# Kernel tuning notes

Measured on AMD Instinct MI355X. Metric: run time of the kernel, lower is better.

Reference implementation:

```python
import jax, jax.numpy as jnp
import numpy as np

HEADS, DH, M_LAND, PINV_ITERS, LN_EPS = 8, 64, 256, 6, 1e-5


def layer_norm(x, g, b):
    mu = x.mean(-1, keepdims=True)
    var = ((x - mu) ** 2).mean(-1, keepdims=True)
    return (x - mu) * jax.lax.rsqrt(var + LN_EPS) * g + b


def moore_penrose_pinv(x, iters=PINV_ITERS):
    # x: (h, m, m). Iterative Newton-Schulz style pinv (lucidrains).
    abs_x = jnp.abs(x)
    col = abs_x.sum(-1)
    row = abs_x.sum(-2)
    z = jnp.swapaxes(x, -1, -2) / (jnp.max(col) * jnp.max(row))
    I = jnp.eye(x.shape[-1], dtype=x.dtype)
    for _ in range(iters):
        xz = x @ z
        z = 0.25 * z @ (13.0 * I - xz @ (15.0 * I - xz @ (7.0 * I - xz)))
    return z


def nystrom_attention(x, qkv_w, out_w, out_b, res_w):
    # x: (n, dim). No mask, eval mode (dropout off).
    n, dim = x.shape
    pad = (-n) % M_LAND
    xp = jnp.pad(x, ((pad, 0), (0, 0)))  # pad at sequence START, as in original
    n_p = n + pad
    l = n_p // M_LAND  # tokens per landmark
    qkv = xp @ qkv_w  # (n_p, 3*h*dh)
    q, k, v = jnp.split(qkv, 3, axis=-1)
    split = lambda t: t.reshape(n_p, HEADS, DH).transpose(1, 0, 2)  # (h, n_p, dh)
    q, k, v = split(q), split(k), split(v)
    q = q * (DH ** -0.5)
    q_l = q.reshape(HEADS, M_LAND, l, DH).mean(axis=2)  # (h, m, dh)
    k_l = k.reshape(HEADS, M_LAND, l, DH).mean(axis=2)
    sim1 = jnp.einsum('hid,hjd->hij', q, k_l)    # (h, n_p, m)
    sim2 = jnp.einsum('hid,hjd->hij', q_l, k_l)  # (h, m, m)
    sim3 = jnp.einsum('hid,hjd->hij', q_l, k)    # (h, m, n_p)
    a1 = jax.nn.softmax(sim1, axis=-1)
    a2 = jax.nn.softmax(sim2, axis=-1)
    a3 = jax.nn.softmax(sim3, axis=-1)
    a2_inv = moore_penrose_pinv(a2)
    out = a1 @ (a2_inv @ (a3 @ v))  # (h, n_p, dh)
    # residual depthwise conv over sequence dim, kernel 33, per head
    res = jax.lax.conv_general_dilated(
        v[None], res_w, (1, 1), ((16, 16), (0, 0)),
        feature_group_count=HEADS, dimension_numbers=('NCHW', 'OIHW', 'NCHW'))[0]
    out = out + res
    out = out.transpose(1, 0, 2).reshape(n_p, HEADS * DH)
    out = out @ out_w + out_b
    return out[-n:]  # drop the leading pad


def ppeg(x, w7, b7, w5, b5, w3, b3, H, W):
    cls_tok, feat = x[0], x[1:]
    C = feat.shape[1]
    img = feat.T.reshape(1, C, H, W)
    def dw(w, b, p):
        y = jax.lax.conv_general_dilated(
            img, w, (1, 1), ((p, p), (p, p)),
            feature_group_count=C, dimension_numbers=('NCHW', 'OIHW', 'NCHW'))
        return y + b.reshape(1, C, 1, 1)
    out = img + dw(w7, b7, 3) + dw(w5, b5, 2) + dw(w3, b3, 1)
    out = out[0].reshape(C, H * W).T
    return jnp.concatenate([cls_tok[None], out], axis=0)


def forward(h, fc1_w, fc1_b, cls_token, l1_ln_g, l1_ln_b, l1_qkv_w, l1_out_w, l1_out_b, l1_res_w,
            conv7_w, conv7_b, conv5_w, conv5_b, conv3_w, conv3_b,
            l2_ln_g, l2_ln_b, l2_qkv_w, l2_out_w, l2_out_b, l2_res_w,
            norm_g, norm_b, fc2_w, fc2_b):
    x = jax.nn.relu(h @ fc1_w + fc1_b)  # (N, 512)
    N = x.shape[0]
    Hs = Ws = int(np.ceil(np.sqrt(N)))  # N chosen perfect square -> add_length == 0
    x = jnp.concatenate([cls_token, x], axis=0)  # (N+1, 512)
    x = x + nystrom_attention(layer_norm(x, l1_ln_g, l1_ln_b), l1_qkv_w, l1_out_w, l1_out_b, l1_res_w)
    x = ppeg(x, conv7_w, conv7_b, conv5_w, conv5_b, conv3_w, conv3_b, Hs, Ws)
    x = x + nystrom_attention(layer_norm(x, l2_ln_g, l2_ln_b), l2_qkv_w, l2_out_w, l2_out_b, l2_res_w)
    x = layer_norm(x, norm_g, norm_b)[0]  # cls token readout
    return x @ fc2_w + fc2_b  # (n_classes,)


def setup_inputs() -> dict:
    key = jax.random.key(0)
    ks = jax.random.split(key, 16)
    nrm = lambda k, s, sc=0.02: jax.random.normal(k, s, jnp.float32) * sc
    D = 512
    return {
        'h': jax.random.normal(ks[0], (16384, 2048), jnp.float32),
        'fc1_w': nrm(ks[1], (2048, D)), 'fc1_b': jnp.zeros((D,), jnp.float32),
        'cls_token': nrm(ks[2], (1, D), 1.0),
        'l1_ln_g': jnp.ones((D,), jnp.float32), 'l1_ln_b': jnp.zeros((D,), jnp.float32),
        'l1_qkv_w': nrm(ks[3], (D, 3 * D)),
        'l1_out_w': nrm(ks[4], (D, D)), 'l1_out_b': jnp.zeros((D,), jnp.float32),
        'l1_res_w': nrm(ks[5], (HEADS, 1, 33, 1), 0.05),
        'conv7_w': nrm(ks[6], (D, 1, 7, 7), 0.05), 'conv7_b': jnp.zeros((D,), jnp.float32),
        'conv5_w': nrm(ks[7], (D, 1, 5, 5), 0.05), 'conv5_b': jnp.zeros((D,), jnp.float32),
        'conv3_w': nrm(ks[8], (D, 1, 3, 3), 0.05), 'conv3_b': jnp.zeros((D,), jnp.float32),
        'l2_ln_g': jnp.ones((D,), jnp.float32), 'l2_ln_b': jnp.zeros((D,), jnp.float32),
        'l2_qkv_w': nrm(ks[9], (D, 3 * D)),
        'l2_out_w': nrm(ks[10], (D, D)), 'l2_out_b': jnp.zeros((D,), jnp.float32),
        'l2_res_w': nrm(ks[11], (HEADS, 1, 33, 1), 0.05),
        'norm_g': jnp.ones((D,), jnp.float32), 'norm_b': jnp.zeros((D,), jnp.float32),
        'fc2_w': nrm(ks[12], (D, 2)), 'fc2_b': jnp.zeros((2,), jnp.float32),
    }


def reference(h, fc1_w, fc1_b, cls_token, l1_ln_g, l1_ln_b, l1_qkv_w, l1_out_w, l1_out_b, l1_res_w,
              conv7_w, conv7_b, conv5_w, conv5_b, conv3_w, conv3_b,
              l2_ln_g, l2_ln_b, l2_qkv_w, l2_out_w, l2_out_b, l2_res_w,
              norm_g, norm_b, fc2_w, fc2_b):
    return forward(h, fc1_w, fc1_b, cls_token, l1_ln_g, l1_ln_b, l1_qkv_w, l1_out_w, l1_out_b, l1_res_w,
                   conv7_w, conv7_b, conv5_w, conv5_b, conv3_w, conv3_b,
                   l2_ln_g, l2_ln_b, l2_qkv_w, l2_out_w, l2_out_b, l2_res_w,
                   norm_g, norm_b, fc2_w, fc2_b)
```

## Files before the change

### kernel.cpp

```cpp
#include <hip/hip_runtime.h>
#include <cstddef>

#define NROWS 16385
#define NPAD  16640
#define PADT  255
#define DIM   512
#define HEADS 8
#define DH    64
#define NL    256
#define LCH   65
#define LCHUNK 52
#define KCH   320
#define SLACK 24
#define LDST  40
#define AST   72

typedef short bf16x8 __attribute__((ext_vector_type(8)));
typedef float f32x4  __attribute__((ext_vector_type(4)));

__device__ __forceinline__ float wsum(float v){
#pragma unroll
  for (int o = 32; o; o >>= 1) v += __shfl_xor(v, o);
  return v;
}
__device__ __forceinline__ float wmax(float v){
#pragma unroll
  for (int o = 32; o; o >>= 1) v = fmaxf(v, __shfl_xor(v, o));
  return v;
}
__device__ __forceinline__ float red16max(float v){
  v = fmaxf(v, __shfl_xor(v, 1));
  v = fmaxf(v, __shfl_xor(v, 2));
  v = fmaxf(v, __shfl_xor(v, 4));
  v = fmaxf(v, __shfl_xor(v, 8));
  return v;
}
__device__ __forceinline__ float red16sum(float v){
  v += __shfl_xor(v, 1);
  v += __shfl_xor(v, 2);
  v += __shfl_xor(v, 4);
  v += __shfl_xor(v, 8);
  return v;
}

__device__ __forceinline__ void split2(float x, unsigned short &h, unsigned short &l){
  unsigned ux = __float_as_uint(x);
  unsigned rh = (ux + 0x7FFFu + ((ux >> 16) & 1u)) >> 16;
  h = (unsigned short)rh;
  float fh = __uint_as_float(rh << 16);
  float r = x - fh;
  unsigned ur = __float_as_uint(r);
  unsigned rl = (ur + 0x7FFFu + ((ur >> 16) & 1u)) >> 16;
  l = (unsigned short)rl;
}
__device__ __forceinline__ float bf2f(unsigned short h){
  return __uint_as_float((unsigned)h << 16);
}

__global__ __launch_bounds__(256) void gemm64_sp_kernel(
    const unsigned short* __restrict__ Ah, const unsigned short* __restrict__ Al,
    const unsigned short* __restrict__ Bth, const unsigned short* __restrict__ Btl,
    const unsigned short* __restrict__ IBh, const unsigned short* __restrict__ IBl,
    float* __restrict__ Cf,
    unsigned short* __restrict__ Crh, unsigned short* __restrict__ Crl,
    unsigned short* __restrict__ Cth, unsigned short* __restrict__ Ctl,
    int M, int N, int K, long sA, long sB, long sC,
    float alpha, float ib)
{
  size_t zo = (size_t)blockIdx.z;
  Ah  += zo*sA; Al  += zo*sA;
  Bth += zo*sB; Btl += zo*sB;
  if (IBh){ IBh += zo*sA; IBl += zo*sA; }
  if (Cf)  Cf  += zo*sC;
  if (Crh){ Crh += zo*sC; Crl += zo*sC; }
  if (Cth){ Cth += zo*sC; Ctl += zo*sC; }
  __shared__ unsigned short LAh[64*LDST], LAl[64*LDST], LBh[64*LDST], LBl[64*LDST];
  const int t = threadIdx.x;
  const int wid = t >> 6, lane = t & 63;
  const int wr = wid >> 1, wc = wid & 1;
  const int l15 = lane & 15, kb = lane >> 4;
  const int bm = blockIdx.y << 6, bn = blockIdx.x << 6;
  const int r4 = t >> 2, kc = (t & 3) << 3;
  f32x4 acc[2][2];
#pragma unroll
  for (int i=0;i<2;++i)
#pragma unroll
    for (int j=0;j<2;++j) acc[i][j] = (f32x4){0.f,0.f,0.f,0.f};

  for (int k0 = 0; k0 < K; k0 += 32){
    __syncthreads();
    {
      int lo = r4*LDST + kc;
      *(uint4*)&LAh[lo] = *(const uint4*)&Ah[(size_t)(bm+r4)*K + k0 + kc];
      *(uint4*)&LAl[lo] = *(const uint4*)&Al[(size_t)(bm+r4)*K + k0 + kc];
      *(uint4*)&LBh[lo] = *(const uint4*)&Bth[(size_t)(bn+r4)*K + k0 + kc];
      *(uint4*)&LBl[lo] = *(const uint4*)&Btl[(size_t)(bn+r4)*K + k0 + kc];
    }
    __syncthreads();
    bf16x8 ah[2], al[2], bh[2], bl[2];
#pragma unroll
    for (int r=0;r<2;++r){
      int off = (wr*32 + r*16 + l15)*LDST + kb*8;
      ah[r] = *(const bf16x8*)&LAh[off];
      al[r] = *(const bf16x8*)&LAl[off];
    }
#pragma unroll
    for (int c2=0;c2<2;++c2){
      int off = (wc*32 + c2*16 + l15)*LDST + kb*8;
      bh[c2] = *(const bf16x8*)&LBh[off];
      bl[c2] = *(const bf16x8*)&LBl[off];
    }
#pragma unroll
    for (int r=0;r<2;++r)
#pragma unroll
      for (int c2=0;c2<2;++c2){
        acc[r][c2] = __builtin_amdgcn_mfma_f32_16x16x32_bf16(ah[r], bh[c2], acc[r][c2], 0,0,0);
        acc[r][c2] = __builtin_amdgcn_mfma_f32_16x16x32_bf16(ah[r], bl[c2], acc[r][c2], 0,0,0);
        acc[r][c2] = __builtin_amdgcn_mfma_f32_16x16x32_bf16(al[r], bh[c2], acc[r][c2], 0,0,0);
      }
  }
#pragma unroll
  for (int r=0;r<2;++r){
#pragma unroll
    for (int c2=0;c2<2;++c2){
      int col = bn + wc*32 + c2*16 + l15;
      int rb  = bm + wr*32 + r*16 + kb*4;
      float v[4];
#pragma unroll
      for (int e=0;e<4;++e){
        float x = acc[r][c2][e];
        if (ib != 0.f){
          size_t io = (size_t)(rb+e)*K + col;
          float ibv = bf2f(IBh[io]) + bf2f(IBl[io]);
          x = alpha*(ib*ibv - x);
        } else {
          x = alpha*x;
        }
        v[e] = x;
      }
      if (Cf){
#pragma unroll
        for (int e=0;e<4;++e) Cf[(size_t)(rb+e)*N + col] = v[e];
      }
      if (Crh){
#pragma unroll
        for (int e=0;e<4;++e){
          unsigned short hh, ll;
          split2(v[e], hh, ll);
          Crh[(size_t)(rb+e)*N + col] = hh;
          Crl[(size_t)(rb+e)*N + col] = ll;
        }
      }
      if (Cth){
        unsigned short h4[4], l4[4];
#pragma unroll
        for (int e=0;e<4;++e) split2(v[e], h4[e], l4[e]);
        uint2 uh, ul;
        uh.x = (unsigned)h4[0] | ((unsigned)h4[1]<<16);
        uh.y = (unsigned)h4[2] | ((unsigned)h4[3]<<16);
        ul.x = (unsigned)l4[0] | ((unsigned)l4[1]<<16);
        ul.y = (unsigned)l4[2] | ((unsigned)l4[3]<<16);
        *(uint2*)&Cth[(size_t)col*M + rb] = uh;
        *(uint2*)&Ctl[(size_t)col*M + rb] = ul;
      }
    }
  }
}

__global__ __launch_bounds__(256) void gemm_sb_kernel(
    const unsigned short* __restrict__ Ah, const unsigned short* __restrict__ Al,
    const unsigned short* __restrict__ BTh, const unsigned short* __restrict__ BTl,
    const float* __restrict__ bias, float* __restrict__ C,
    int M, int N, int K, int accum)
{
  __shared__ unsigned short LAh[128*LDST], LAl[128*LDST], LBh[128*LDST], LBl[128*LDST];
  const int t = threadIdx.x;
  const int bm = blockIdx.y << 7, bn = blockIdx.x << 7;
  const int wid = t >> 6, lane = t & 63;
  const int wr = wid >> 1, wc = wid & 1;
  const int l15 = lane & 15, kb = lane >> 4;
  const int sr = t >> 1, sc0 = (t & 1) << 4;
  f32x4 acc[4][4];
#pragma unroll
  for (int i=0;i<4;++i)
#pragma unroll
    for (int j=0;j<4;++j) acc[i][j] = (f32x4){0.f,0.f,0.f,0.f};

  const uint4 zz = make_uint4(0,0,0,0);
  for (int k0 = 0; k0 < K; k0 += 32){
    __syncthreads();
    {
      bool av = (bm + sr) < M;
      size_t ga = (size_t)(bm + sr)*K + k0 + sc0;
      uint4 a0 = av ? *(const uint4*)(Ah + ga)     : zz;
// ... 153 lines not shown
}

__global__ void att_split_kernel(const float* __restrict__ ATT,
                                 unsigned short* __restrict__ Ah,
                                 unsigned short* __restrict__ Al)
{
  size_t i4 = (size_t)blockIdx.x*256 + threadIdx.x;
  size_t e = i4*4;
  int row = (int)(e >> 9);
  float4 v = make_float4(0.f,0.f,0.f,0.f);
  if (row < NROWS) v = *(const float4*)(ATT + (size_t)PADT*DIM + e);
  unsigned short h0,l0,h1,l1,h2,l2,h3,l3;
  split2(v.x,h0,l0); split2(v.y,h1,l1); split2(v.z,h2,l2); split2(v.w,h3,l3);
  uint2 uh, ul;
  uh.x = (unsigned)h0 | ((unsigned)h1<<16); uh.y = (unsigned)h2 | ((unsigned)h3<<16);
  ul.x = (unsigned)l0 | ((unsigned)l1<<16); ul.y = (unsigned)l2 | ((unsigned)l3<<16);
  *(uint2*)(Ah + e) = uh;
  *(uint2*)(Al + e) = ul;
}

__global__ __launch_bounds__(256) void ln_pad_sb_kernel(
    const float* __restrict__ X, const float* __restrict__ g,
    const float* __restrict__ b, unsigned short* __restrict__ Yh,
    unsigned short* __restrict__ Yl)
{
  int p = blockIdx.x;
  int t = threadIdx.x;
  size_t base = (size_t)p*DIM;
  if (p < PADT){
    Yh[base+t] = 0; Yh[base+t+256] = 0;
    Yl[base+t] = 0; Yl[base+t+256] = 0;
    return;
  }
  const float* xr = X + (size_t)(p-PADT)*DIM;
  float x0 = xr[t], x1 = xr[t+256];
  float s = x0 + x1, sq = x0*x0 + x1*x1;
  s = wsum(s); sq = wsum(sq);
  __shared__ float rs[4], rq[4];
  if ((t&63)==0){ rs[t>>6]=s; rq[t>>6]=sq; }
  __syncthreads();
  float S = rs[0]+rs[1]+rs[2]+rs[3];
  float SQ = rq[0]+rq[1]+rq[2]+rq[3];
  float mu = S * (1.f/DIM);
  float var = SQ * (1.f/DIM) - mu*mu;
  float r = rsqrtf(var + 1e-5f);
  float y0 = (x0-mu)*r*g[t]     + b[t];
  float y1 = (x1-mu)*r*g[t+256] + b[t+256];
  unsigned short h, l;
  split2(y0, h, l); Yh[base+t] = h;     Yl[base+t] = l;
  split2(y1, h, l); Yh[base+t+256] = h; Yl[base+t+256] = l;
}

__global__ void landmarks_kernel(const float* __restrict__ QKV,
                                 float* __restrict__ QL, float* __restrict__ KL)
{
  int m = blockIdx.x, h = blockIdx.y, d = threadIdx.x;
  float sq = 0.f, sk = 0.f;
  const float* base = QKV + (size_t)(m*LCH)*1536 + (h<<6) + d;
  for (int j = 0; j < LCH; ++j){
    sq += base[0];
    sk += base[512];
    base += 1536;
  }
  QL[(((h<<8)+m)<<6) + d] = sq * (0.125f/65.f);
  KL[(((h<<8)+m)<<6) + d] = sk * (1.f/65.f);
}

__global__ void klsplit_kernel(const float* __restrict__ KL,
                               unsigned short* __restrict__ KLh,
                               unsigned short* __restrict__ KLl)
{
  int i = blockIdx.x*256 + threadIdx.x;
  unsigned short h, l;
  split2(KL[i], h, l);
  KLh[i] = h; KLl[i] = l;
}

__global__ __launch_bounds__(256) void sim2_kernel(
    const float* __restrict__ QL, const float* __restrict__ KL, float* __restrict__ A2)
{
  int m = blockIdx.x, h = blockIdx.y, n = threadIdx.x;
  __shared__ float ql[64];
  __shared__ float red[4];
  if (n < 64) ql[n] = QL[(((h<<8)+m)<<6) + n];
  __syncthreads();
  const float* kl = KL + (size_t)(((h<<8)+n)<<6);
  float s = 0.f;
#pragma unroll
  for (int d=0; d<64; ++d) s += ql[d]*kl[d];
  float mx = wmax(s);
  if ((n&63)==0) red[n>>6] = mx;
  __syncthreads();
  mx = fmaxf(fmaxf(red[0],red[1]), fmaxf(red[2],red[3]));
  float e = __expf(s - mx);
  float sm = wsum(e);
  __syncthreads();
  if ((n&63)==0) red[n>>6] = sm;
  __syncthreads();
  sm = red[0]+red[1]+red[2]+red[3];
  A2[((size_t)((h<<8)+m)<<8) + n] = e/sm;
}

__global__ void crsum_kernel(const float* __restrict__ A2, float* __restrict__ CR)
{
  int b = blockIdx.x, t = threadIdx.x;
  float v;
  if (b < 2048){
    v = fabsf(A2[((size_t)b<<8) + t]);
  } else {
    int r = b - 2048;
    int h = r >> 8, n = r & 255;
    v = fabsf(A2[((size_t)h<<16) + (t<<8) + n]);
  }
  v = wsum(v);
  __shared__ float red[4];
  if ((t&63)==0) red[t>>6]=v;
  __syncthreads();
  if (t==0) CR[b] = red[0]+red[1]+red[2]+red[3];
}
__global__ void maxprod_kernel(const float* __restrict__ CR, float* __restrict__ SCAL)
{
  int t = threadIdx.x;
  float mc = -3e38f, mr = -3e38f;
  for (int i=t; i<2048; i+=256){ mc = fmaxf(mc, CR[i]); mr = fmaxf(mr, CR[2048+i]); }
  mc = wmax(mc); mr = wmax(mr);
  __shared__ float rc[4], rr[4];
  if ((t&63)==0){ rc[t>>6]=mc; rr[t>>6]=mr; }
  __syncthreads();
  if (t==0){
    float a = fmaxf(fmaxf(rc[0],rc[1]),fmaxf(rc[2],rc[3]));
    float b = fmaxf(fmaxf(rr[0],rr[1]),fmaxf(rr[2],rr[3]));
    SCAL[0] = 1.f/(a*b);
  }
}

__global__ void tsplit_kernel(const float* __restrict__ A2, const float* __restrict__ SCAL,
                              unsigned short* __restrict__ A2h, unsigned short* __restrict__ A2l,
                              unsigned short* __restrict__ Zrh, unsigned short* __restrict__ Zrl,
                              unsigned short* __restrict__ Zth, unsigned short* __restrict__ Ztl)
{
  int idx = blockIdx.x*256 + threadIdx.x;
  int h = idx >> 16, rem = idx & 65535, m = rem >> 8, n = rem & 255;
  float a = A2[idx];
  unsigned short hh, ll;
  split2(a, hh, ll);
  A2h[idx] = hh; A2l[idx] = ll;
  float z = a * SCAL[0];
  split2(z, hh, ll);
  Zth[idx] = hh; Ztl[idx] = ll;
  size_t rmo = ((size_t)h<<16) + (n<<8) + m;
  Zrh[rmo] = hh; Zrl[rmo] = ll;
}

__global__ __launch_bounds__(256) void lattn2_kernel(
    const float* __restrict__ QKV, const float* __restrict__ QL,
    float* __restrict__ PACC, float* __restrict__ PML)
{
  const int c = blockIdx.x, lg = blockIdx.y, h = blockIdx.z;
  const int t = threadIdx.x, tx = t & 15, ty = t >> 4;
  __shared__ float QLs[64][68], KtsPs[64][68], Vs[64][68];
  {
    int r = t >> 2, c0 = (t & 3) << 4;
    const float* src = QL + (((size_t)((h << 8) + (lg << 6) + r)) << 6) + c0;
#pragma unroll
    for (int q = 0; q < 4; ++q)
      *(float4*)&QLs[r][c0 + (q<<2)] = ((const float4*)src)[q];
  }
  float M[4], L[4], acc[4][4];
#pragma unroll
  for (int i = 0; i < 4; ++i){
    M[i] = -3e38f; L[i] = 0.f;
#pragma unroll
    for (int j = 0; j < 4; ++j) acc[i][j] = 0.f;
  }
  const int key = t & 63, kd0 = (t >> 6) << 4;
  const int vr = t >> 2, vc = (t & 3) << 4;
  for (int s = 0; s < 5; ++s){
    const int j0 = c * KCH + (s << 6);
    __syncthreads();
    {
      const float* kp = QKV + (size_t)(j0 + key) * 1536 + 512 + (h << 6) + kd0;
#pragma unroll
      for (int q = 0; q < 4; ++q){
        float4 kv = ((const float4*)kp)[q];
        KtsPs[kd0 + (q<<2) + 0][key] = kv.x;
        KtsPs[kd0 + (q<<2) + 1][key] = kv.y;
        KtsPs[kd0 + (q<<2) + 2][key] = kv.z;
        KtsPs[kd0 + (q<<2) + 3][key] = kv.w;
      }
      const float* vp = QKV + (size_t)(j0 + vr) * 1536 + 1024 + (h << 6) + vc;
#pragma unroll
      for (int q = 0; q < 4; ++q)
        *(float4*)&Vs[vr][vc + (q<<2)] = ((const float4*)vp)[q];
    }
    __syncthreads();
    float sv[4][4];
#pragma unroll
    for (int i=0;i<4;++i)
#pragma unroll
      for (int j=0;j<4;++j) sv[i][j] = 0.f;
    for (int d = 0; d < 64; d += 4){
      float a[4][4], b[4][4];
#pragma unroll
      for (int i = 0; i < 4; ++i)
        *(float4*)a[i] = *(const float4*)&QLs[(ty<<2)+i][d];
#pragma unroll
      for (int dd = 0; dd < 4; ++dd)
        *(float4*)b[dd] = *(const float4*)&KtsPs[d+dd][tx<<2];
#pragma unroll
      for (int i = 0; i < 4; ++i)
#pragma unroll
        for (int dd = 0; dd < 4; ++dd){
          float av = a[i][dd];
#pragma unroll
          for (int j = 0; j < 4; ++j) sv[i][j] += av * b[dd][j];
        }
    }
#pragma unroll
    for (int i = 0; i < 4; ++i){
      float rm = fmaxf(fmaxf(sv[i][0], sv[i][1]), fmaxf(sv[i][2], sv[i][3]));
      rm = red16max(rm);
      float Mn = fmaxf(M[i], rm);
      float sc = __expf(M[i] - Mn);
      float rs = 0.f;
#pragma unroll
      for (int j = 0; j < 4; ++j){
        float p = __expf(sv[i][j] - Mn);
        sv[i][j] = p; rs += p;
      }
      rs = red16sum(rs);
      L[i] = L[i] * sc + rs;
      M[i] = Mn;
#pragma unroll
      for (int j = 0; j < 4; ++j) acc[i][j] *= sc;
    }
    __syncthreads();
#pragma unroll
    for (int i = 0; i < 4; ++i)
      *(float4*)&KtsPs[(ty<<2)+i][tx<<2] = *(float4*)sv[i];
    for (int k = 0; k < 64; k += 4){
      float a[4][4], b[4][4];
#pragma unroll
      for (int i = 0; i < 4; ++i)
        *(float4*)a[i] = *(const float4*)&KtsPs[(ty<<2)+i][k];
#pragma unroll
      for (int kk = 0; kk < 4; ++kk)
        *(float4*)b[kk] = *(const float4*)&Vs[k+kk][tx<<2];
#pragma unroll
      for (int i = 0; i < 4; ++i)
#pragma unroll
        for (int kk = 0; kk < 4; ++kk){
          float av = a[i][kk];
#pragma unroll
          for (int j = 0; j < 4; ++j) acc[i][j] += av * b[kk][j];
        }
    }
  }
  size_t base = (size_t)(c * 8 + h) * 256 + (lg << 6) + (ty << 2);
#pragma unroll
  for (int i = 0; i < 4; ++i)
    *(float4*)&PACC[(base + i) * 64 + (tx << 2)] = *(float4*)acc[i];
  if (tx == 0){
#pragma unroll
    for (int i = 0; i < 4; ++i){
      PML[(base + i) * 2 + 0] = M[i];
      PML[(base + i) * 2 + 1] = L[i];
    }
  }
}

__global__ void lattn_combine_kernel(const float* __restrict__ PACC,
                                     const float* __restrict__ PML,
                                     unsigned short* __restrict__ TMth,
                                     unsigned short* __restrict__ TMtl)
{
  int hm = blockIdx.x, d = threadIdx.x;
  int h = hm >> 8, m = hm & 255;
  float Mg = -3e38f;
#pragma unroll
  for (int c = 0; c < LCHUNK; ++c){
    size_t b = ((size_t)(c * 8 + h) * 256 + m) * 2;
    Mg = fmaxf(Mg, PML[b]);
  }
  float Sg = 0.f, o = 0.f;
#pragma unroll 4
  for (int c = 0; c < LCHUNK; ++c){
    size_t b = ((size_t)(c * 8 + h) * 256 + m) * 2;
    float e = __expf(PML[b] - Mg);
    Sg += PML[b+1] * e;
    o += PACC[((size_t)(c * 8 + h) * 256 + m) * 64 + d] * e;
  }
  unsigned short hh, ll;
  split2(o / Sg, hh, ll);
  size_t off = (size_t)h*16384 + (size_t)d*256 + m;
  TMth[off] = hh; TMtl[off] = ll;
}

__global__ __launch_bounds__(256) void attn3_kernel(
    const float* __restrict__ QKV,
    const unsigned short* __restrict__ KLh, const unsigned short* __restrict__ KLl,
    const unsigned short* __restrict__ BMth, const unsigned short* __restrict__ BMtl,
    float* __restrict__ ATT)
{
  const int qb = blockIdx.x, h = blockIdx.y;
  const int t = threadIdx.x;
  const int w = t >> 6, lane = t & 63;
  const int l15 = lane & 15, kb = lane >> 4;
  __shared__ unsigned short LQh[64*AST], LQl[64*AST];
  __shared__ unsigned short LAh[64*AST], LAl[64*AST];
  __shared__ unsigned short LPh[64*AST], LPl[64*AST];
  {
    int r = t >> 2, kc = (t & 3) << 4;
    int row = qb*64 + r; if (row > NROWS-1) row = NROWS-1;
    const float* qp = QKV + (size_t)(PADT+row)*1536 + (h<<6) + kc;
    float va[16];
    *(float4*)&va[0]  = ((const float4*)qp)[0];
    *(float4*)&va[4]  = ((const float4*)qp)[1];
    *(float4*)&va[8]  = ((const float4*)qp)[2];
    *(float4*)&va[12] = ((const float4*)qp)[3];
    unsigned* dh = (unsigned*)&LQh[r*AST + kc];
    unsigned* dl = (unsigned*)&LQl[r*AST + kc];
#pragma unroll
    for (int q=0;q<8;++q){
      unsigned short h0,l0,h1,l1;
      split2(va[2*q]*0.125f,   h0, l0);
      split2(va[2*q+1]*0.125f, h1, l1);
      dh[q] = (unsigned)h0 | ((unsigned)h1 << 16);
      dl[q] = (unsigned)l0 | ((unsigned)l1 << 16);
    }
  }
  float m = -3e38f, l = 0.f;
  f32x4 oacc[4];
#pragma unroll
  for (int i=0;i<4;++i) oacc[i] = (f32x4){0.f,0.f,0.f,0.f};
  const int sr = t >> 2, sc0 = (t & 3) << 4;

  for (int lt = 0; lt < 4; ++lt){
    __syncthreads();
    {
      size_t g = ((size_t)(h*256 + lt*64 + sr))*64 + sc0;
      uint4 vh0 = *(const uint4*)&KLh[g];
      uint4 vh1 = *(const uint4*)&KLh[g+8];
      uint4 vl0 = *(const uint4*)&KLl[g];
      uint4 vl1 = *(const uint4*)&KLl[g+8];
      int lo = sr*AST + sc0;
      *(uint4*)&LAh[lo]   = vh0;
      *(uint4*)&LAh[lo+8] = vh1;
      *(uint4*)&LAl[lo]   = vl0;
      *(uint4*)&LAl[lo+8] = vl1;
    }
    __syncthreads();
    f32x4 sacc[4];
#pragma unroll
    for (int i=0;i<4;++i) sacc[i] = (f32x4){0.f,0.f,0.f,0.f};
#pragma unroll
    for (int ks = 0; ks < 2; ++ks){
      int qoff = (w*16 + l15)*AST + ks*32 + kb*8;
      bf16x8 bh = *(const bf16x8*)&LQh[qoff];
      bf16x8 bl = *(const bf16x8*)&LQl[qoff];
#pragma unroll
      for (int mi=0; mi<4; ++mi){
        int aoff = (mi*16 + l15)*AST + ks*32 + kb*8;
        bf16x8 ah = *(const bf16x8*)&LAh[aoff];
        bf16x8 al = *(const bf16x8*)&LAl[aoff];
        sacc[mi] = __builtin_amdgcn_mfma_f32_16x16x32_bf16(ah, bh, sacc[mi], 0,0,0);
        sacc[mi] = __builtin_amdgcn_mfma_f32_16x16x32_bf16(ah, bl, sacc[mi], 0,0,0);
        sacc[mi] = __builtin_amdgcn_mfma_f32_16x16x32_bf16(al, bh, sacc[mi], 0,0,0);
      }
    }
    float tm = -3e38f;
#pragma unroll
    for (int mi=0;mi<4;++mi)
#pragma unroll
      for (int e=0;e<4;++e) tm = fmaxf(tm, sacc[mi][e]);
    tm = fmaxf(tm, __shfl_xor(tm, 16));
    tm = fmaxf(tm, __shfl_xor(tm, 32));
    float Mn = fmaxf(m, tm);
    float sc = __expf(m - Mn);
    float ts = 0.f;
    float p[4][4];
#pragma unroll
    for (int mi=0;mi<4;++mi)
#pragma unroll
      for (int e=0;e<4;++e){
        float pv = __expf(sacc[mi][e] - Mn);
        p[mi][e] = pv; ts += pv;
      }
    ts += __shfl_xor(ts, 16);
    ts += __shfl_xor(ts, 32);
    l = l*sc + ts;
    m = Mn;
#pragma unroll
    for (int mi=0;mi<4;++mi)
#pragma unroll
      for (int e=0;e<4;++e) oacc[mi][e] *= sc;
#pragma unroll
    for (int mi=0;mi<4;++mi){
      unsigned short h4[4], l4[4];
#pragma unroll
      for (int e=0;e<4;++e) split2(p[mi][e], h4[e], l4[e]);
      uint2 uh, ul;
      uh.x = (unsigned)h4[0] | ((unsigned)h4[1]<<16);
      uh.y = (unsigned)h4[2] | ((unsigned)h4[3]<<16);
      ul.x = (unsigned)l4[0] | ((unsigned)l4[1]<<16);
      ul.y = (unsigned)l4[2] | ((unsigned)l4[3]<<16);
      int po = (w*16 + l15)*AST + mi*16 + kb*4;
      *(uint2*)&LPh[po] = uh;
      *(uint2*)&LPl[po] = ul;
    }
    __syncthreads();
    {
      size_t g = ((size_t)(h*64 + sr))*256 + lt*64 + sc0;
      uint4 vh0 = *(const uint4*)&BMth[g];
      uint4 vh1 = *(const uint4*)&BMth[g+8];
      uint4 vl0 = *(const uint4*)&BMtl[g];
      uint4 vl1 = *(const uint4*)&BMtl[g+8];
      int lo = sr*AST + sc0;
      *(uint4*)&LAh[lo]   = vh0;
      *(uint4*)&LAh[lo+8] = vh1;
      *(uint4*)&LAl[lo]   = vl0;
// ... 60 lines not shown
  }
#pragma unroll
  for (int k=0;k<4;++k){
    int i = i0 + k;
    if (i < NPAD) ATT[(size_t)i*DIM + c] += acc[k];
  }
}

__global__ void pad_kernel(const float* __restrict__ X, float* __restrict__ PIM)
{
  int r = blockIdx.x;
  int c = blockIdx.y*256 + threadIdx.x;
  int py = r / 134, px = r - py*134;
  float v = 0.f;
  if (py>=3 && py<131 && px>=3 && px<131)
    v = X[(size_t)(1 + (py-3)*128 + (px-3))*512 + c];
  PIM[(size_t)r*512 + c] = v;
}

__global__ void wtrans_kernel(const float* __restrict__ w7, const float* __restrict__ w5,
                              const float* __restrict__ w3, float* __restrict__ W7T,
                              float* __restrict__ W5T, float* __restrict__ W3T)
{
  int i = blockIdx.x;
  int c = blockIdx.y*256 + threadIdx.x;
  if (i < 49)      W7T[i*512+c]      = w7[c*49+i];
  else if (i < 74) W5T[(i-49)*512+c] = w5[c*25+(i-49)];
  else             W3T[(i-74)*512+c] = w3[c*9+(i-74)];
}

__global__ __launch_bounds__(256) void ppeg2_kernel(
    const float* __restrict__ PIM, const float* __restrict__ W7T,
    const float* __restrict__ W5T, const float* __restrict__ W3T,
    const float* __restrict__ b7, const float* __restrict__ b5,
    const float* __restrict__ b3, float* __restrict__ X2)
{
  const int t = threadIdx.x;
  const int c = blockIdx.z*256 + t;
  const int x = blockIdx.x;
  const int y0 = blockIdx.y << 2;
  float w7r[49], w5r[25], w3r[9];
#pragma unroll
  for (int i=0;i<49;++i) w7r[i] = W7T[i*512 + c];
#pragma unroll
  for (int i=0;i<25;++i) w5r[i] = W5T[i*512 + c];
#pragma unroll
  for (int i=0;i<9;++i)  w3r[i] = W3T[i*512 + c];
  const float bsum = b7[c] + b5[c] + b3[c];
  float acc[4] = {bsum, bsum, bsum, bsum};
  const float* base = PIM + ((size_t)(y0*134 + x))*512 + c;
#pragma unroll
  for (int rr=0; rr<10; ++rr){
#pragma unroll
    for (int cc=0; cc<7; ++cc){
      float v = base[(size_t)(rr*134 + cc)*512];
#pragma unroll
      for (int k=0;k<4;++k){
        const int dy = rr - k - 3, dx = cc - 3;
        if (dy >= -3 && dy <= 3){
          acc[k] += w7r[(dy+3)*7 + (dx+3)] * v;
          if (dy >= -2 && dy <= 2 && dx >= -2 && dx <= 2)
            acc[k] += w5r[(dy+2)*5 + (dx+2)] * v;
          if (dy >= -1 && dy <= 1 && dx >= -1 && dx <= 1)
            acc[k] += w3r[(dy+1)*3 + (dx+1)] * v;
          if (dy == 0 && dx == 0) acc[k] += v;
        }
      }
    }
  }
#pragma unroll
  for (int k=0;k<4;++k)
    X2[(size_t)(1 + (y0+k)*128 + x)*512 + c] = acc[k];
}

__global__ void copy_row_kernel(const float* __restrict__ src, float* __restrict__ dst)
{
  dst[threadIdx.x] = src[threadIdx.x];
}

__global__ void final_kernel(const float* __restrict__ X, const float* __restrict__ g,
                             const float* __restrict__ b, const float* __restrict__ fw,
                             const float* __restrict__ fb, float* __restrict__ out)
{
  int t = threadIdx.x;
  float x0 = X[t], x1 = X[t+256];
  float s = x0 + x1, sq = x0*x0 + x1*x1;
  s = wsum(s); sq = wsum(sq);
  __shared__ float rs[4], rq[4];
  if ((t&63)==0){ rs[t>>6]=s; rq[t>>6]=sq; }
  __syncthreads();
  float S = rs[0]+rs[1]+rs[2]+rs[3];
  float SQ = rq[0]+rq[1]+rq[2]+rq[3];
  float mu = S*(1.f/DIM);
  float var = SQ*(1.f/DIM) - mu*mu;
  float r = rsqrtf(var + 1e-5f);
  float n0 = (x0-mu)*r*g[t]     + b[t];
  float n1 = (x1-mu)*r*g[t+256] + b[t+256];
  float p0 = n0*fw[t*2]   + n1*fw[(t+256)*2];
  float p1 = n0*fw[t*2+1] + n1*fw[(t+256)*2+1];
  p0 = wsum(p0); p1 = wsum(p1);
  __shared__ float r0[4], r1[4];
  if ((t&63)==0){ r0[t>>6]=p0; r1[t>>6]=p1; }
  __syncthreads();
  if (t==0){
    out[0] = r0[0]+r0[1]+r0[2]+r0[3] + fb[0];
    out[1] = r1[0]+r1[1]+r1[2]+r1[3] + fb[1];
  }
}

struct Bufs {
  float *Y, *QKV, *QL, *KL, *A2, *CR, *SCAL, *PACC, *PML, *W7T, *W5T, *W3T;
  unsigned short *Yh, *Yl, *ATh, *ATl, *qBTh, *qBTl, *oBTh, *oBTl, *fBTh, *fBTl;
  unsigned short *A2h, *A2l, *XZrh, *XZrl, *XZth, *XZtl, *Wth, *Wtl, *W2th, *W2tl;
  unsigned short *Z0rh, *Z0rl, *Z0th, *Z0tl, *Z1rh, *Z1rl, *Z1th, *Z1tl;
  unsigned short *TMth, *TMtl, *KLh, *KLl, *BMth, *BMtl;
};

static void attention_layer(float* X, const float* ln_g, const float* ln_b,
                            const float* qkv_w, const float* out_w, const float* out_b,
                            const float* res_w, Bufs& bf, hipStream_t stream)
{
  const long SP = 65536;
  wt_split_T_kernel<<<(1536*512)/256, 256, 0, stream>>>(qkv_w, bf.qBTh, bf.qBTl, 512, 1536);
  wt_split_T_kernel<<<(512*512)/256, 256, 0, stream>>>(out_w, bf.oBTh, bf.oBTl, 512, 512);
  ln_pad_sb_kernel<<<NPAD, 256, 0, stream>>>(X, ln_g, ln_b, bf.Yh, bf.Yl);
  gemm_sb_kernel<<<dim3(12,130),256,0,stream>>>(bf.Yh, bf.Yl, bf.qBTh, bf.qBTl,
      nullptr, bf.QKV, NPAD, 1536, 512, 0);
  landmarks_kernel<<<dim3(NL,HEADS),64,0,stream>>>(bf.QKV, bf.QL, bf.KL);
  klsplit_kernel<<<512,256,0,stream>>>(bf.KL, bf.KLh, bf.KLl);
  sim2_kernel<<<dim3(NL,HEADS),256,0,stream>>>(bf.QL, bf.KL, bf.A2);
  crsum_kernel<<<4096,256,0,stream>>>(bf.A2, bf.CR);
  maxprod_kernel<<<1,256,0,stream>>>(bf.CR, bf.SCAL);
  tsplit_kernel<<<2048,256,0,stream>>>(bf.A2, bf.SCAL, bf.A2h, bf.A2l,
      bf.Z0rh, bf.Z0rl, bf.Z0th, bf.Z0tl);
  unsigned short *Zarh=bf.Z0rh, *Zarl=bf.Z0rl, *Zath=bf.Z0th, *Zatl=bf.Z0tl;
  unsigned short *Zbrh=bf.Z1rh, *Zbrl=bf.Z1rl, *Zbth=bf.Z1th, *Zbtl=bf.Z1tl;
  for (int it = 0; it < 6; ++it){
    gemm64_sp_kernel<<<dim3(4,4,8),256,0,stream>>>(bf.A2h, bf.A2l, Zath, Zatl,
        nullptr, nullptr, nullptr, bf.XZrh, bf.XZrl, bf.XZth, bf.XZtl,
        256,256,256, SP,SP,SP, 1.f, 0.f);
    gemm64_sp_kernel<<<dim3(4,4,8),256,0,stream>>>(bf.XZrh, bf.XZrl, bf.XZth, bf.XZtl,
        bf.XZrh, bf.XZrl, nullptr, nullptr, nullptr, bf.Wth, bf.Wtl,
        256,256,256, SP,SP,SP, 1.f, 7.f);
    gemm64_sp_kernel<<<dim3(4,4,8),256,0,stream>>>(bf.XZrh, bf.XZrl, bf.Wth, bf.Wtl,
        bf.XZrh, bf.XZrl, nullptr, nullptr, nullptr, bf.W2th, bf.W2tl,
        256,256,256, SP,SP,SP, 1.f, 15.f);
    gemm64_sp_kernel<<<dim3(4,4,8),256,0,stream>>>(Zarh, Zarl, bf.W2th, bf.W2tl,
        Zarh, Zarl, nullptr, Zbrh, Zbrl, Zbth, Zbtl,
        256,256,256, SP,SP,SP, 0.25f, 13.f);
    unsigned short* tp;
    tp=Zarh; Zarh=Zbrh; Zbrh=tp;  tp=Zarl; Zarl=Zbrl; Zbrl=tp;
    tp=Zath; Zath=Zbth; Zbth=tp;  tp=Zatl; Zatl=Zbtl; Zbtl=tp;
  }
  lattn2_kernel<<<dim3(LCHUNK,4,HEADS),256,0,stream>>>(bf.QKV, bf.QL, bf.PACC, bf.PML);
  lattn_combine_kernel<<<2048,64,0,stream>>>(bf.PACC, bf.PML, bf.TMth, bf.TMtl);
  gemm64_sp_kernel<<<dim3(1,4,8),256,0,stream>>>(Zarh, Zarl, bf.TMth, bf.TMtl,
      nullptr, nullptr, nullptr, nullptr, nullptr, bf.BMth, bf.BMtl,
      256,64,256, SP, 16384L, 16384L, 1.f, 0.f);
  float* ATT = bf.Y;
  attn3_kernel<<<dim3(257,HEADS),256,0,stream>>>(bf.QKV, bf.KLh, bf.KLl,
      bf.BMth, bf.BMtl, ATT);
  convres2_kernel<<<dim3(4097,2),256,0,stream>>>(bf.QKV, res_w, ATT);
  att_split_kernel<<<8256,256,0,stream>>>(ATT, bf.ATh, bf.ATl);
  gemm_sb_kernel<<<dim3(4,129),256,0,stream>>>(bf.ATh, bf.ATl, bf.oBTh, bf.oBTl,
      out_b, X, NROWS, 512, 512, 1);
}

extern "C" void kernel_launch(void* const* d_in, const int* in_sizes, int n_in,
                              void* d_out, int out_size, void* d_ws, size_t ws_size,
                              hipStream_t stream)
{
  (void)in_sizes; (void)n_in; (void)out_size; (void)ws_size;
  const float* h       = (const float*)d_in[0];
  const float* fc1_w   = (const float*)d_in[1];
  const float* fc1_b   = (const float*)d_in[2];
  const float* cls     = (const float*)d_in[3];
  const float* l1_ln_g = (const float*)d_in[4];
  const float* l1_ln_b = (const float*)d_in[5];
  const float* l1_qkv_w= (const float*)d_in[6];
  const float* l1_out_w= (const float*)d_in[7];
  const float* l1_out_b= (const float*)d_in[8];
  const float* l1_res_w= (const float*)d_in[9];
  const float* conv7_w = (const float*)d_in[10];
  const float* conv7_b = (const float*)d_in[11];
  const float* conv5_w = (const float*)d_in[12];
  const float* conv5_b = (const float*)d_in[13];
  const float* conv3_w = (const float*)d_in[14];
  const float* conv3_b = (const float*)d_in[15];
  const float* l2_ln_g = (const float*)d_in[16];
  const float* l2_ln_b = (const float*)d_in[17];
  const float* l2_qkv_w= (const float*)d_in[18];
  const float* l2_out_w= (const float*)d_in[19];
  const float* l2_out_b= (const float*)d_in[20];
  const float* l2_res_w= (const float*)d_in[21];
  const float* norm_g  = (const float*)d_in[22];
  const float* norm_b  = (const float*)d_in[23];
  const float* fc2_w   = (const float*)d_in[24];
  const float* fc2_b   = (const float*)d_in[25];

  float* ws = (float*)d_ws;
  float* X   = ws;                 ws += (size_t)NROWS*DIM;
  float* X2  = ws;                 ws += (size_t)NROWS*DIM;
  Bufs bf;
  bf.Y    = ws;                    ws += (size_t)NPAD*DIM;
  bf.QKV  = ws;                    ws += (size_t)(NPAD+SLACK)*1536;
  bf.QL   = ws;                    ws += HEADS*NL*DH;
  bf.KL   = ws;                    ws += HEADS*NL*DH;
  bf.A2   = ws;                    ws += HEADS*NL*NL;
  bf.CR   = ws;                    ws += 4096;
  bf.SCAL = ws;                    ws += 8;
  bf.PACC = ws;                    ws += (size_t)LCHUNK*HEADS*NL*DH;
  bf.PML  = ws;                    ws += (size_t)LCHUNK*HEADS*NL*2;
  bf.W7T  = ws;                    ws += 49*512;
  bf.W5T  = ws;                    ws += 25*512;
  bf.W3T  = ws;                    ws += 9*512;
  unsigned short* us = (unsigned short*)ws;
  bf.Yh   = us;                    us += (size_t)NPAD*DIM;
  bf.Yl   = us;                    us += (size_t)NPAD*DIM;
  bf.ATh  = us;                    us += (size_t)16512*DIM;
  bf.ATl  = us;                    us += (size_t)16512*DIM;
  bf.qBTh = us;                    us += 1536*512;
  bf.qBTl = us;                    us += 1536*512;
  bf.oBTh = us;                    us += 512*512;
  bf.oBTl = us;                    us += 512*512;
  bf.fBTh = us;                    us += 512*2048;
  bf.fBTl = us;                    us += 512*2048;
  const size_t PL = (size_t)HEADS*NL*NL;
  bf.A2h  = us; us += PL;  bf.A2l  = us; us += PL;
  bf.XZrh = us; us += PL;  bf.XZrl = us; us += PL;
  bf.XZth = us; us += PL;  bf.XZtl = us; us += PL;
  bf.Wth  = us; us += PL;  bf.Wtl  = us; us += PL;
  bf.W2th = us; us += PL;  bf.W2tl = us; us += PL;
  bf.Z0rh = us; us += PL;  bf.Z0rl = us; us += PL;
  bf.Z0th = us; us += PL;  bf.Z0tl = us; us += PL;
  bf.Z1rh = us; us += PL;  bf.Z1rl = us; us += PL;
  bf.Z1th = us; us += PL;  bf.Z1tl = us; us += PL;
  bf.TMth = us; us += (size_t)HEADS*NL*DH;
  bf.TMtl = us; us += (size_t)HEADS*NL*DH;
  bf.KLh  = us; us += (size_t)HEADS*NL*DH;
  bf.KLl  = us; us += (size_t)HEADS*NL*DH;
  bf.BMth = us; us += (size_t)HEADS*NL*DH;
  bf.BMtl = us; us += (size_t)HEADS*NL*DH;
  float* PIM = bf.QKV;

  zero_slack_kernel<<<(SLACK*1536)/256, 256, 0, stream>>>(bf.QKV);
  wtrans_kernel<<<dim3(83,2),256,0,stream>>>(conv7_w, conv5_w, conv3_w,
                                             bf.W7T, bf.W5T, bf.W3T);

  wt_split_T_kernel<<<(512*2048)/256, 256, 0, stream>>>(fc1_w, bf.fBTh, bf.fBTl, 2048, 512);
  gemm_sbf_kernel<<<dim3(4,128),256,0,stream>>>(h, bf.fBTh, bf.fBTl, fc1_b, X + DIM,
      16384, 512, 2048, 1);
  copy_row_kernel<<<1,512,0,stream>>>(cls, X);

  attention_layer(X, l1_ln_g, l1_ln_b, l1_qkv_w, l1_out_w, l1_out_b, l1_res_w, bf, stream);

  pad_kernel<<<dim3(17956,2),256,0,stream>>>(X, PIM);
  ppeg2_kernel<<<dim3(128,32,2),256,0,stream>>>(PIM, bf.W7T, bf.W5T, bf.W3T,
                                                conv7_b, conv5_b, conv3_b, X2);
  copy_row_kernel<<<1,512,0,stream>>>(X, X2);

  attention_layer(X2, l2_ln_g, l2_ln_b, l2_qkv_w, l2_out_w, l2_out_b, l2_res_w, bf, stream);

  final_kernel<<<1,256,0,stream>>>(X2, norm_g, norm_b, fc2_w, fc2_b, (float*)d_out);
}
```

Before: 2.038 ms.

## Rewrite landmark-key attention with split-bf16 MFMA and 256-key chunks

Replaces the scalar fp32 FMA landmark-query over all-keys attention kernel with an MFMA version. Q, K, V and the probabilities are split into hi/lo bf16 pairs and multiplied with three MFMAs to approximate fp32 accuracy. Each block now covers 256 keys in four 64-key steps, and the chunk count rises from 52 to 65 to match. The kernel adds split overhead, a transposed V store into shared memory, and more partials for the combine kernel to read, in exchange for using matrix cores.

Result: faster. 1.943 ms (-4.7%).

```diff
diff --git a/kernel.cpp b/kernel.cpp
--- a/kernel.cpp
+++ b/kernel.cpp
@@ -9,8 +9,7 @@
 #define DH    64
 #define NL    256
 #define LCH   65
-#define LCHUNK 52
-#define KCH   320
+#define LCHUNK 65
 #define SLACK 24
 #define LDST  40
 #define AST   72
@@ -26,20 +25,6 @@
 __device__ __forceinline__ float wmax(float v){
 #pragma unroll
   for (int o = 32; o; o >>= 1) v = fmaxf(v, __shfl_xor(v, o));
-  return v;
-}
-__device__ __forceinline__ float red16max(float v){
-  v = fmaxf(v, __shfl_xor(v, 1));
-  v = fmaxf(v, __shfl_xor(v, 2));
-  v = fmaxf(v, __shfl_xor(v, 4));
-  v = fmaxf(v, __shfl_xor(v, 8));
-  return v;
-}
-__device__ __forceinline__ float red16sum(float v){
-  v += __shfl_xor(v, 1);
-  v += __shfl_xor(v, 2);
-  v += __shfl_xor(v, 4);
-  v += __shfl_xor(v, 8);
   return v;
 }
 
@@ -499,120 +484,164 @@
   Zrh[rmo] = hh; Zrl[rmo] = ll;
 }
 
-__global__ __launch_bounds__(256) void lattn2_kernel(
+__global__ __launch_bounds__(256) void lattn3_kernel(
     const float* __restrict__ QKV, const float* __restrict__ QL,
     float* __restrict__ PACC, float* __restrict__ PML)
 {
   const int c = blockIdx.x, lg = blockIdx.y, h = blockIdx.z;
-  const int t = threadIdx.x, tx = t & 15, ty = t >> 4;
-  __shared__ float QLs[64][68], KtsPs[64][68], Vs[64][68];
+  const int t = threadIdx.x;
+  const int w = t >> 6, lane = t & 63;
+  const int l15 = lane & 15, kb = lane >> 4;
+  __shared__ unsigned short LQh[64*AST], LQl[64*AST];
+  __shared__ unsigned short LKh[64*AST], LKl[64*AST];
+  __shared__ unsigned short LPh[64*AST], LPl[64*AST];
+  const int sr = t >> 2, sc0 = (t & 3) << 4;
   {
-    int r = t >> 2, c0 = (t & 3) << 4;
-    const float* src = QL + (((size_t)((h << 8) + (lg << 6) + r)) << 6) + c0;
-#pragma unroll
-    for (int q = 0; q < 4; ++q)
-      *(float4*)&QLs[r][c0 + (q<<2)] = ((const float4*)src)[q];
-  }
-  float M[4], L[4], acc[4][4];
-#pragma unroll
-  for (int i = 0; i < 4; ++i){
-    M[i] = -3e38f; L[i] = 0.f;
-#pragma unroll
-    for (int j = 0; j < 4; ++j) acc[i][j] = 0.f;
-  }
-  const int key = t & 63, kd0 = (t >> 6) << 4;
-  const int vr = t >> 2, vc = (t & 3) << 4;
-  for (int s = 0; s < 5; ++s){
-    const int j0 = c * KCH + (s << 6);
+    const float* qp = QL + (((size_t)(h*256 + lg*64 + sr)) << 6) + sc0;
+    float va[16];
+    *(float4*)&va[0]  = ((const float4*)qp)[0];
+    *(float4*)&va[4]  = ((const float4*)qp)[1];
+    *(float4*)&va[8]  = ((const float4*)qp)[2];
+    *(float4*)&va[12] = ((const float4*)qp)[3];
+    unsigned* dh = (unsigned*)&LQh[sr*AST + sc0];
+    unsigned* dl = (unsigned*)&LQl[sr*AST + sc0];
+#pragma unroll
+    for (int q=0;q<8;++q){
+      unsigned short h0,l0,h1,l1;
+      split2(va[2*q],   h0, l0);
+      split2(va[2*q+1], h1, l1);
+      dh[q] = (unsigned)h0 | ((unsigned)h1 << 16);
+      dl[q] = (unsigned)l0 | ((unsigned)l1 << 16);
+    }
+  }
+  float m = -3e38f, l = 0.f;
+  f32x4 oacc[4];
+#pragma unroll
+  for (int i=0;i<4;++i) oacc[i] = (f32x4){0.f,0.f,0.f,0.f};
+
+  for (int s = 0; s < 4; ++s){
+    const int kbase = c*256 + s*64;
     __syncthreads();
     {
-      const float* kp = QKV + (size_t)(j0 + key) * 1536 + 512 + (h << 6) + kd0;
-#pragma unroll
-      for (int q = 0; q < 4; ++q){
-        float4 kv = ((const float4*)kp)[q];
-        KtsPs[kd0 + (q<<2) + 0][key] = kv.x;
-        KtsPs[kd0 + (q<<2) + 1][key] = kv.y;
-        KtsPs[kd0 + (q<<2) + 2][key] = kv.z;
-        KtsPs[kd0 + (q<<2) + 3][key] = kv.w;
-      }
-      const float* vp = QKV + (size_t)(j0 + vr) * 1536 + 1024 + (h << 6) + vc;
-#pragma unroll
-      for (int q = 0; q < 4; ++q)
-        *(float4*)&Vs[vr][vc + (q<<2)] = ((const float4*)vp)[q];
-    }
-    __syncthreads();
-    float sv[4][4];
-#pragma unroll
-    for (int i=0;i<4;++i)
-#pragma unroll
-      for (int j=0;j<4;++j) sv[i][j] = 0.f;
-    for (int d = 0; d < 64; d += 4){
-      float a[4][4], b[4][4];
-#pragma unroll
-      for (int i = 0; i < 4; ++i)
-        *(float4*)a[i] = *(const float4*)&QLs[(ty<<2)+i][d];
-#pragma unroll
-      for (int dd = 0; dd < 4; ++dd)
-        *(float4*)b[dd] = *(const float4*)&KtsPs[d+dd][tx<<2];
-#pragma unroll
-      for (int i = 0; i < 4; ++i)
-#pragma unroll
-        for (int dd = 0; dd < 4; ++dd){
-          float av = a[i][dd];
-#pragma unroll
-          for (int j = 0; j < 4; ++j) sv[i][j] += av * b[dd][j];
-        }
-    }
-#pragma unroll
-    for (int i = 0; i < 4; ++i){
-      float rm = fmaxf(fmaxf(sv[i][0], sv[i][1]), fmaxf(sv[i][2], sv[i][3]));
-      rm = red16max(rm);
-      float Mn = fmaxf(M[i], rm);
-      float sc = __expf(M[i] - Mn);
-      float rs = 0.f;
-#pragma unroll
-      for (int j = 0; j < 4; ++j){
-        float p = __expf(sv[i][j] - Mn);
-        sv[i][j] = p; rs += p;
-      }
-      rs = red16sum(rs);
-      L[i] = L[i] * sc + rs;
-      M[i] = Mn;
-#pragma unroll
-      for (int j = 0; j < 4; ++j) acc[i][j] *= sc;
-    }
-    __syncthreads();
-#pragma unroll
-    for (int i = 0; i < 4; ++i)
-      *(float4*)&KtsPs[(ty<<2)+i][tx<<2] = *(float4*)sv[i];
-    for (int k = 0; k < 64; k += 4){
-      float a[4][4], b[4][4];
-#pragma unroll
-      for (int i = 0; i < 4; ++i)
-        *(float4*)a[i] = *(const float4*)&KtsPs[(ty<<2)+i][k];
-#pragma unroll
-      for (int kk = 0; kk < 4; ++kk)
-        *(float4*)b[kk] = *(const float4*)&Vs[k+kk][tx<<2];
-#pragma unroll
-      for (int i = 0; i < 4; ++i)
-#pragma unroll
-        for (int kk = 0; kk < 4; ++kk){
-          float av = a[i][kk];
-#pragma unroll
-          for (int j = 0; j < 4; ++j) acc[i][j] += av * b[kk][j];
-        }
-    }
-  }
-  size_t base = (size_t)(c * 8 + h) * 256 + (lg << 6) + (ty << 2);
-#pragma unroll
-  for (int i = 0; i < 4; ++i)
-    *(float4*)&PACC[(base + i) * 64 + (tx << 2)] = *(float4*)acc[i];
-  if (tx == 0){
-#pragma unroll
-    for (int i = 0; i < 4; ++i){
-      PML[(base + i) * 2 + 0] = M[i];
-      PML[(base + i) * 2 + 1] = L[i];
-    }
+      const float* kp = QKV + (size_t)(kbase + sr)*1536 + 512 + (h<<6) + sc0;
+      float va[16];
+      *(float4*)&va[0]  = ((const float4*)kp)[0];
+      *(float4*)&va[4]  = ((const float4*)kp)[1];
+      *(float4*)&va[8]  = ((const float4*)kp)[2];
+      *(float4*)&va[12] = ((const float4*)kp)[3];
+      unsigned* dh = (unsigned*)&LKh[sr*AST + sc0];
+      unsigned* dl = (unsigned*)&LKl[sr*AST + sc0];
+#pragma unroll
+      for (int q=0;q<8;++q){
+        unsigned short h0,l0,h1,l1;
+        split2(va[2*q],   h0, l0);
+        split2(va[2*q+1], h1, l1);
+        dh[q] = (unsigned)h0 | ((unsigned)h1 << 16);
+        dl[q] = (unsigned)l0 | ((unsigned)l1 << 16);
+      }
+    }
+    __syncthreads();
+    f32x4 sacc[4];
+#pragma unroll
+    for (int i=0;i<4;++i) sacc[i] = (f32x4){0.f,0.f,0.f,0.f};
+#pragma unroll
+    for (int ks = 0; ks < 2; ++ks){
+      int qoff = (w*16 + l15)*AST + ks*32 + kb*8;
+      bf16x8 bh = *(const bf16x8*)&LQh[qoff];
+      bf16x8 bl = *(const bf16x8*)&LQl[qoff];
+#pragma unroll
+      for (int mi=0; mi<4; ++mi){
+        int aoff = (mi*16 + l15)*AST + ks*32 + kb*8;
+        bf16x8 ah = *(const bf16x8*)&LKh[aoff];
+        bf16x8 al = *(const bf16x8*)&LKl[aoff];
+        sacc[mi] = __builtin_amdgcn_mfma_f32_16x16x32_bf16(ah, bh, sacc[mi], 0,0,0);
+        sacc[mi] = __builtin_amdgcn_mfma_f32_16x16x32_bf16(ah, bl, sacc[mi], 0,0,0);
+        sacc[mi] = __builtin_amdgcn_mfma_f32_16x16x32_bf16(al, bh, sacc[mi], 0,0,0);
+      }
+    }
+    float tm = -3e38f;
+#pragma unroll
+    for (int mi=0;mi<4;++mi)
+#pragma unroll
+      for (int e=0;e<4;++e) tm = fmaxf(tm, sacc[mi][e]);
+    tm = fmaxf(tm, __shfl_xor(tm, 16));
+    tm = fmaxf(tm, __shfl_xor(tm, 32));
+    float Mn = fmaxf(m, tm);
+    float sc = __expf(m - Mn);
+    float ts = 0.f;
+    float p[4][4];
+#pragma unroll
+    for (int mi=0;mi<4;++mi)
+#pragma unroll
+      for (int e=0;e<4;++e){
+        float pv = __expf(sacc[mi][e] - Mn);
+        p[mi][e] = pv; ts += pv;
+      }
+    ts += __shfl_xor(ts, 16);
+    ts += __shfl_xor(ts, 32);
+    l = l*sc + ts;
+    m = Mn;
+#pragma unroll
+    for (int mi=0;mi<4;++mi)
+#pragma unroll
+      for (int e=0;e<4;++e) oacc[mi][e] *= sc;
+#pragma unroll
+    for (int mi=0;mi<4;++mi){
+      unsigned short h4[4], l4[4];
+#pragma unroll
+      for (int e=0;e<4;++e) split2(p[mi][e], h4[e], l4[e]);
+      uint2 uh, ul;
+      uh.x = (unsigned)h4[0] | ((unsigned)h4[1]<<16);
+      uh.y = (unsigned)h4[2] | ((unsigned)h4[3]<<16);
+      ul.x = (unsigned)l4[0] | ((unsigned)l4[1]<<16);
+      ul.y = (unsigned)l4[2] | ((unsigned)l4[3]<<16);
+      int po = (w*16 + l15)*AST + mi*16 + kb*4;
+      *(uint2*)&LPh[po] = uh;
+      *(uint2*)&LPl[po] = ul;
+    }
+    __syncthreads();
+    {
+      const float* vp = QKV + (size_t)(kbase + sr)*1536 + 1024 + (h<<6) + sc0;
+      float va[16];
+      *(float4*)&va[0]  = ((const float4*)vp)[0];
+      *(float4*)&va[4]  = ((const float4*)vp)[1];
+      *(float4*)&va[8]  = ((const float4*)vp)[2];
+      *(float4*)&va[12] = ((const float4*)vp)[3];
+#pragma unroll
+      for (int i=0;i<16;++i){
+        unsigned short hh, ll;
+        split2(va[i], hh, ll);
+        LKh[(sc0+i)*AST + sr] = hh;
+        LKl[(sc0+i)*AST + sr] = ll;
+      }
+    }
+    __syncthreads();
+#pragma unroll
+    for (int ks = 0; ks < 2; ++ks){
+      int poff = (w*16 + l15)*AST + ks*32 + kb*8;
+      bf16x8 pbh = *(const bf16x8*)&LPh[poff];
+      bf16x8 pbl = *(const bf16x8*)&LPl[poff];
+#pragma unroll
+      for (int mi=0; mi<4; ++mi){
+        int aoff = (mi*16 + l15)*AST + ks*32 + kb*8;
+        bf16x8 ah = *(const bf16x8*)&LKh[aoff];
+        bf16x8 al = *(const bf16x8*)&LKl[aoff];
+        oacc[mi] = __builtin_amdgcn_mfma_f32_16x16x32_bf16(ah, pbh, oacc[mi], 0,0,0);
+        oacc[mi] = __builtin_amdgcn_mfma_f32_16x16x32_bf16(ah, pbl, oacc[mi], 0,0,0);
+        oacc[mi] = __builtin_amdgcn_mfma_f32_16x16x32_bf16(al, pbh, oacc[mi], 0,0,0);
+      }
+    }
+  }
+  size_t row = (size_t)(c*8 + h)*256 + lg*64 + w*16 + l15;
+#pragma unroll
+  for (int mi=0;mi<4;++mi){
+    float4 o;
+    o.x = oacc[mi][0]; o.y = oacc[mi][1]; o.z = oacc[mi][2]; o.w = oacc[mi][3];
+    *(float4*)&PACC[row*64 + mi*16 + kb*4] = o;
+  }
+  if (kb == 0){
+    PML[row*2 + 0] = m;
+    PML[row*2 + 1] = l;
   }
 }
 
@@ -979,7 +1008,7 @@
     tp=Zarh; Zarh=Zbrh; Zbrh=tp;  tp=Zarl; Zarl=Zbrl; Zbrl=tp;
     tp=Zath; Zath=Zbth; Zbth=tp;  tp=Zatl; Zatl=Zbtl; Zbtl=tp;
   }
-  lattn2_kernel<<<dim3(LCHUNK,4,HEADS),256,0,stream>>>(bf.QKV, bf.QL, bf.PACC, bf.PML);
+  lattn3_kernel<<<dim3(LCHUNK,4,HEADS),256,0,stream>>>(bf.QKV, bf.QL, bf.PACC, bf.PML);
   lattn_combine_kernel<<<2048,64,0,stream>>>(bf.PACC, bf.PML, bf.TMth, bf.TMtl);
   gemm64_sp_kernel<<<dim3(1,4,8),256,0,stream>>>(Zarh, Zarl, bf.TMth, bf.TMtl,
       nullptr, nullptr, nullptr, nullptr, nullptr, bf.BMth, bf.BMtl,
```
